# Performance work log

Measured on AMD Instinct MI355X. Metric: run time of the kernel, lower is better.

## Reference

```python
import jax, jax.numpy as jnp
import numpy as np

KER = 8  # patch size used by unfold/fold
EPS = 1e-5


def _gelu(x):
    return jax.nn.gelu(x, approximate=False)  # torch nn.GELU default (exact erf)


def _conv(x, w, b):
    # x: [B,C,H,W], w: [O,I,kh,kw]
    y = jax.lax.conv_general_dilated(x, w, (1, 1), 'SAME',
                                     dimension_numbers=('NCHW', 'OIHW', 'NCHW'))
    return y + b[None, :, None, None]


def _unfold_t(x):
    # F.unfold(k=8, s=8).transpose(1,2): [B,C,H,W] -> [B, L, C*k*k]
    B, C, H, W = x.shape
    Hp, Wp = H // KER, W // KER
    x = x.reshape(B, C, Hp, KER, Wp, KER)
    x = x.transpose(0, 2, 4, 1, 3, 5)  # [B,Hp,Wp,C,k,k]
    return x.reshape(B, Hp * Wp, C * KER * KER)


def _fold(y, H, W):
    # inverse of unfold (non-overlapping): [B,L,C*k*k] -> [B,C,H,W]
    B, L, D = y.shape
    Hp, Wp = H // KER, W // KER
    C = D // (KER * KER)
    y = y.reshape(B, Hp, Wp, C, KER, KER).transpose(0, 3, 1, 4, 2, 5)
    return y.reshape(B, C, H, W)


def _bn1d(x, gamma, beta):
    # BatchNorm1d (training-mode batch stats) on [B, C, L]: stats over (B, L)
    m = x.mean(axis=(0, 2), keepdims=True)
    v = x.var(axis=(0, 2), keepdims=True)  # biased variance, matches torch fwd
    return (x - m) * jax.lax.rsqrt(v + EPS) * gamma[None, :, None] + beta[None, :, None]


def setup_inputs() -> dict:
    key = jax.random.key(0)
    ks = jax.random.split(key, 12)
    B, C, H, W = 4, 64, 256, 256
    dq = KER * KER * C  # 4096

    def n(k, shape, scale=0.02):
        return jax.random.normal(k, shape, jnp.float32) * scale

    return {
        'feat': jax.random.normal(ks[0], (B, C, H, W), jnp.float32),
        'w_enc': n(ks[1], (C, C, 3, 3)), 'b_enc': jnp.zeros((C,), jnp.float32),
        'w_kc': n(ks[2], (C, C, 3, 3)), 'b_kc': jnp.zeros((C,), jnp.float32),
        'w_vc': n(ks[3], (C, C, 3, 3)), 'b_vc': jnp.zeros((C,), jnp.float32),
        'wq': n(ks[4], (1024, dq)), 'bq': jnp.zeros((1024,), jnp.float32),
        'wk': n(ks[5], (1024, dq)), 'bk': jnp.zeros((1024,), jnp.float32),
        'gq': jnp.ones((1024,), jnp.float32), 'betaq': jnp.zeros((1024,), jnp.float32),
        'gk': jnp.ones((1024,), jnp.float32), 'betak': jnp.zeros((1024,), jnp.float32),
        'w_f1': n(ks[6], (4 * C, C, 1, 1)), 'b_f1': jnp.zeros((4 * C,), jnp.float32),
        'w_f2': n(ks[7], (C, 4 * C, 1, 1)), 'b_f2': jnp.zeros((C,), jnp.float32),
    }


def reference(feat, w_enc, b_enc, w_kc, b_kc, w_vc, b_vc, wq, bq, wk, bk,
              gq, betaq, gk, betak, w_f1, b_f1, w_f2, b_f2):
    H, W = feat.shape[-2:]
    refer = _gelu(_conv(feat, w_enc, b_enc))
    feat_k = _gelu(_conv(feat, w_kc, b_kc))
    feat_v = _gelu(_conv(feat, w_vc, b_vc))

    q_un = _unfold_t(refer)   # [B,L,4096]
    k_un = _unfold_t(feat_k)
    v_un = _unfold_t(feat_v)

    # Linear -> BN1d over 1024 channels (transpose dance as in the torch code)
    qp = _bn1d((q_un @ wq.T + bq).transpose(0, 2, 1), gq, betaq).transpose(0, 2, 1)  # [B,L,1024]
    kp = _bn1d((k_un @ wk.T + bk).transpose(0, 2, 1), gk, betak).transpose(0, 2, 1)  # [B,L,1024]

    scale = jnp.sqrt(jnp.asarray(qp.shape[2], qp.dtype))
    scores = jnp.einsum('bld,bmd->blm', qp, kp) / scale  # [B,L,L]
    attn = jax.nn.softmax(scores, axis=2)
    out = jnp.einsum('blm,bmd->bld', attn, v_un)  # [B,L,4096]

    out = _fold(out, H, W)  # [B,C,H,W]
    ff = _gelu(_conv(out, w_f1, b_f1))
    ff = _gelu(_conv(ff, w_f2, b_f2))
    return ff + feat
```

## Files before the change

### kernel.cpp

```cpp
#include <hip/hip_runtime.h>
#include <hip/hip_bf16.h>

typedef unsigned short u16;
typedef __attribute__((ext_vector_type(8))) short short8v;
typedef __attribute__((ext_vector_type(8))) unsigned short u16x8;
typedef __attribute__((ext_vector_type(4))) float f32x4;

#define HWPIX 65536
#define AS1(p) ((const __attribute__((address_space(1))) void*)(p))
#define AS3(p) ((__attribute__((address_space(3))) void*)(p))

__device__ __forceinline__ float bfbits2f(u16 u) {
  return __uint_as_float(((unsigned)u) << 16);
}
__device__ __forceinline__ float4 ld4bf(const u16* p) {
  ushort4 u = *(const ushort4*)(const void*)p;
  return make_float4(bfbits2f(u.x), bfbits2f(u.y), bfbits2f(u.z), bfbits2f(u.w));
}
__device__ __forceinline__ u16 f2bf(float f) {
  union { __hip_bfloat16 h; u16 u; } c;
  c.h = __float2bfloat16(f);
  return c.u;
}
__device__ __forceinline__ float gelu_f(float x) {
  float z = 0.79788456f * x * (1.0f + 0.044715f * x * x);
  float e = __expf(2.0f * z);
  float th = 1.0f - 2.0f * __builtin_amdgcn_rcpf(e + 1.0f);
  return 0.5f * x * (1.0f + th);
}
__device__ __forceinline__ u16x8 bn8(u16x8 v, const float* __restrict__ sc,
                                     const float* __restrict__ sh, int kk) {
  float4 s0 = *(const float4*)&sc[kk], s1 = *(const float4*)&sc[kk + 4];
  float4 t0 = *(const float4*)&sh[kk], t1 = *(const float4*)&sh[kk + 4];
  u16x8 r;
  r[0] = f2bf(bfbits2f(v[0]) * s0.x + t0.x); r[1] = f2bf(bfbits2f(v[1]) * s0.y + t0.y);
  r[2] = f2bf(bfbits2f(v[2]) * s0.z + t0.z); r[3] = f2bf(bfbits2f(v[3]) * s0.w + t0.w);
  r[4] = f2bf(bfbits2f(v[4]) * s1.x + t1.x); r[5] = f2bf(bfbits2f(v[5]) * s1.y + t1.y);
  r[6] = f2bf(bfbits2f(v[6]) * s1.z + t1.z); r[7] = f2bf(bfbits2f(v[7]) * s1.w + t1.w);
  return r;
}

__launch_bounds__(256)
__global__ void nhwc_k(const float* __restrict__ x, u16* __restrict__ y) {
  __shared__ float tile[64][65];
  const int t = threadIdx.x;
  const int xs = blockIdx.x << 6, yy = blockIdx.y, b = blockIdx.z;
#pragma unroll
  for (int it = 0; it < 4; ++it) {
    const int idx = t + it * 256;
    const int c = idx >> 4, seg = (idx & 15) << 2;
    float4 v = *(const float4*)&x[(((size_t)(b * 64 + c)) << 16) + yy * 256 + xs + seg];
    tile[c][seg] = v.x; tile[c][seg + 1] = v.y; tile[c][seg + 2] = v.z; tile[c][seg + 3] = v.w;
  }
  __syncthreads();
#pragma unroll
  for (int it = 0; it < 4; ++it) {
    const int idx = t + it * 256;
    const int cs = (idx & 15) << 2, px = idx >> 4;
    ushort4 r;
    r.x = f2bf(tile[cs + 0][px]); r.y = f2bf(tile[cs + 1][px]);
    r.z = f2bf(tile[cs + 2][px]); r.w = f2bf(tile[cs + 3][px]);
    *(ushort4*)&y[(((size_t)((b * 256 + yy) * 256 + xs + px)) << 6) + cs] = r;
  }
}

__launch_bounds__(256)
__global__ void wcvt2_k(const float* __restrict__ s0, u16* __restrict__ d0,
                        const float* __restrict__ s1, u16* __restrict__ d1) {
  const float* src = blockIdx.y ? s1 : s0;
  u16* dst = blockIdx.y ? d1 : d0;
  const int i = (blockIdx.x * 256 + threadIdx.x) << 2;
  float4 v = *(const float4*)&src[i];
  ushort4 r;
  r.x = f2bf(v.x); r.y = f2bf(v.y); r.z = f2bf(v.z); r.w = f2bf(v.w);
  *(ushort4*)&dst[i] = r;
}

__launch_bounds__(256)
__global__ void wprep_k(const float* __restrict__ w0, const float* __restrict__ w1,
                        const float* __restrict__ w2, const float* __restrict__ b0,
                        const float* __restrict__ b1, const float* __restrict__ b2,
                        const float* __restrict__ wf1, const float* __restrict__ wf2,
                        u16* __restrict__ wT, float* __restrict__ bias192,
                        u16* __restrict__ wf1b, u16* __restrict__ wf2b) {
  const int t = threadIdx.x;
  const int bx = blockIdx.x;
  if (bx >= 497) {
    const int e = (bx - 497) * 256 + t;
    wf2b[e] = f2bf(wf2[e]);
    return;
  }
  if (bx >= 433) {
    const int e = (bx - 433) * 256 + t;
    wf1b[e] = f2bf(wf1[e]);
    return;
  }
  if (bx == 432) {
    if (t < 192) {
      const float* bp = (t < 64) ? b0 : (t < 128) ? b1 : b2;
      bias192[t] = bp[t & 63];
    }
    return;
  }
  const int e = bx * 256 + t;
  const int pos = e / 12288, rem = e % 12288;
  const int n = rem >> 6, ic = rem & 63;
  const int conv = n >> 6, oc = n & 63;
  const float* wp = (conv == 0) ? w0 : (conv == 1) ? w1 : w2;
  wT[e] = f2bf(wp[(oc * 64 + ic) * 9 + pos]);
}

__launch_bounds__(256)
__global__ void convmfma_k(const u16* __restrict__ featb, const u16* __restrict__ wT,
                           const float* __restrict__ bias192, u16* __restrict__ qun,
                           u16* __restrict__ kun, u16* __restrict__ vT) {
  __shared__ u16 As[128 * 64];
  __shared__ u16 Bs[192 * 64];
  const int tid = threadIdx.x;
  const int lin = blockIdx.x;
  const int virt = (lin & 7) * 256 + (lin >> 3);
  const int b = virt >> 9, yy = (virt >> 1) & 255, x0 = (virt & 1) << 7;
  const int lane = tid & 63, w = tid >> 6;
  const int wm = w >> 1, wn = w & 1;

  f32x4 acc[4][6] = {};
  const int kc = (lane >> 4) << 3;
  const int afr = wm * 64 + (lane & 15);
  const int bfr0 = wn * 96 + (lane & 15);

  for (int pos = 0; pos < 9; ++pos) {
    const int dy = pos / 3, dx = pos % 3;
    const int yp = yy + dy - 1;
    const bool yok = (unsigned)yp < 256u;
#pragma unroll
    for (int i = 0; i < 4; ++i) {
      const int slot = tid + (i << 8);
      const int row = slot >> 3, cg = slot & 7;
      const int xp = x0 + row + dx - 1;
      u16x8 v{};
      if (yok && (unsigned)xp < 256u)
        v = *(const u16x8*)&featb[(((size_t)((b * 256 + yp) * 256 + xp)) << 6) + (cg << 3)];
      *(u16x8*)&As[(row << 6) + ((cg ^ (row & 7)) << 3)] = v;
    }
    {
      const u16* wb = wT + (size_t)pos * 12288;
#pragma unroll
      for (int i = 0; i < 6; ++i) {
        const int slot = tid + (i << 8);
        const int row = slot >> 3, cg = slot & 7;
        *(u16x8*)&Bs[(row << 6) + ((cg ^ (row & 7)) << 3)] =
            *(const u16x8*)&wb[(row << 6) + (cg << 3)];
      }
    }
    __syncthreads();
#pragma unroll
    for (int ks = 0; ks < 2; ++ks) {
      const int ce = (ks << 5) + kc;
      short8v a[4], bf[6];
#pragma unroll
      for (int f = 0; f < 4; ++f) {
        const int row = afr + f * 16;
        a[f] = *(const short8v*)&As[(row << 6) + (ce ^ ((row & 7) << 3))];
      }
#pragma unroll
      for (int f = 0; f < 6; ++f) {
        const int row = bfr0 + f * 16;
        bf[f] = *(const short8v*)&Bs[(row << 6) + (ce ^ ((row & 7) << 3))];
      }
#pragma unroll
      for (int i = 0; i < 4; ++i)
#pragma unroll
        for (int j = 0; j < 6; ++j)
          acc[i][j] = __builtin_amdgcn_mfma_f32_16x16x32_bf16(a[i], bf[j], acc[i][j], 0, 0, 0);
    }
    __syncthreads();
  }

  const int py = yy >> 3, ky = yy & 7;
  const int rp0 = wm * 64 + ((lane >> 4) << 2);
#pragma unroll
  for (int j = 0; j < 6; ++j) {
    const int colb = wn * 96 + j * 16;
    const int conv = colb >> 6;
    const int oc = (colb & 63) + (lane & 15);
    const float bj = bias192[colb + (lane & 15)];
#pragma unroll
    for (int i = 0; i < 4; ++i) {
      const int rp = rp0 + i * 16;
      const int xg = x0 + rp;
      const int px = xg >> 3, kx0 = xg & 7;
      float v0 = gelu_f(acc[i][j][0] + bj);
      float v1 = gelu_f(acc[i][j][1] + bj);
      float v2 = gelu_f(acc[i][j][2] + bj);
      float v3 = gelu_f(acc[i][j][3] + bj);
      const int d0 = (oc << 6) + (ky << 3) + kx0;
      if (conv < 2) {
        u16* dst = conv ? kun : qun;
        const size_t addr = (((size_t)((b << 10) + py * 32 + px)) << 12) + d0;
        ushort4 r4;
        r4.x = f2bf(v0); r4.y = f2bf(v1); r4.z = f2bf(v2); r4.w = f2bf(v3);
        *(ushort4*)&dst[addr] = r4;
      } else {
        const int m = py * 32 + px;
        const size_t base = (((size_t)(b * 4096 + d0)) << 10) + m;
        vT[base] = f2bf(v0);
        vT[base + 1024] = f2bf(v1);
        vT[base + 2048] = f2bf(v2);
        vT[base + 3072] = f2bf(v3);
      }
    }
  }
}

__launch_bounds__(256)
__global__ void bnpart_k(const u16* __restrict__ q, const u16* __restrict__ k,
                         float2* __restrict__ part) {
  const u16* x = blockIdx.y ? k : q;
  const int b = blockIdx.x, t = threadIdx.x;
  const int c = t << 2;
  float s0 = 0.f, s1 = 0.f, s2 = 0.f, s3 = 0.f;
  float q0 = 0.f, q1 = 0.f, q2 = 0.f, q3 = 0.f;
  const u16* base = x + ((size_t)b << 15) + c;
#pragma unroll 4
  for (int r = 0; r < 32; ++r) {
    float4 v = ld4bf(base + (r << 10));
    s0 += v.x; q0 += v.x * v.x;
    s1 += v.y; q1 += v.y * v.y;
    s2 += v.z; q2 += v.z * v.z;
    s3 += v.w; q3 += v.w * v.w;
  }
  float2* dst = part + (((size_t)(blockIdx.y * 128 + b)) << 10) + c;
  dst[0] = make_float2(s0, q0);
  dst[1] = make_float2(s1, q1);
  dst[2] = make_float2(s2, q2);
  dst[3] = make_float2(s3, q3);
}
__launch_bounds__(256)
__global__ void bnfin_k(const float2* __restrict__ part, const float* __restrict__ gq,
                        const float* __restrict__ betaq, const float* __restrict__ gk,
                        const float* __restrict__ betak, float* __restrict__ scq,
                        float* __restrict__ shq, float* __restrict__ sck,
                        float* __restrict__ shk) {
  const int n = blockIdx.x * 256 + threadIdx.x;
  const int y = blockIdx.y;
  const float2* p = part + (((size_t)(y * 128)) << 10) + n;
  float S = 0.f, S2 = 0.f;
  for (int i = 0; i < 128; ++i) {
    float2 v = p[(size_t)i << 10];
    S += v.x; S2 += v.y;
  }
  const float mean = S * (1.0f / 4096.0f);
  const float var = S2 * (1.0f / 4096.0f) - mean * mean;
  const float rstd = rsqrtf(var + 1e-5f);
  const float g = (y ? gk : gq)[n];
  const float be = (y ? betak : betaq)[n];
  const float sc = g * rstd;
  (y ? sck : scq)[n] = sc;
  (y ? shk : shq)[n] = be - mean * sc;
}

__launch_bounds__(256)
__global__ void softmax_k(u16* __restrict__ s) {
  u16* p = s + (size_t)blockIdx.x * 1024;
  const int tid = threadIdx.x;
  float4 v = ld4bf(p + (tid << 2));
  float mx = fmaxf(fmaxf(v.x, v.y), fmaxf(v.z, v.w));
#pragma unroll
  for (int off = 32; off > 0; off >>= 1) mx = fmaxf(mx, __shfl_xor(mx, off));
  __shared__ float red[8];
  if ((tid & 63) == 0) red[tid >> 6] = mx;
  __syncthreads();
  mx = fmaxf(fmaxf(red[0], red[1]), fmaxf(red[2], red[3]));
  float e0 = __expf(v.x - mx), e1 = __expf(v.y - mx), e2 = __expf(v.z - mx), e3 = __expf(v.w - mx);
  float sm = e0 + e1 + e2 + e3;
#pragma unroll
  for (int off = 32; off > 0; off >>= 1) sm += __shfl_xor(sm, off);
  if ((tid & 63) == 0) red[4 + (tid >> 6)] = sm;
  __syncthreads();
  sm = red[4] + red[5] + red[6] + red[7];
  float inv = 1.0f / sm;
  ushort4 r;
  r.x = f2bf(e0 * inv); r.y = f2bf(e1 * inv); r.z = f2bf(e2 * inv); r.w = f2bf(e3 * inv);
  *(ushort4*)&p[tid << 2] = r;
}

template <int MODE>
__launch_bounds__(512)
__global__ void mgemmL_k(const u16* __restrict__ Ap0, const u16* __restrict__ Bp0,
                         const float* __restrict__ bias0, u16* __restrict__ Cp0, int K,
                         const u16* __restrict__ Ap2, const u16* __restrict__ Bp2,
                         const float* __restrict__ bias2, u16* __restrict__ Cp2) {
  constexpr int SD = (MODE == 0) ? 4096 : 1024;
  __shared__ u16 As[2][128 * 64];
  __shared__ u16 Bs[2][128 * 64];
  const int tid = threadIdx.x;

  int bx, by, z;
  if constexpr (MODE == 2) {
    int lin = blockIdx.x + 32 * blockIdx.y + 256 * blockIdx.z;
    int sw = (lin & 7) * 128 + (lin >> 3);
    bx = sw & 31; by = (sw >> 5) & 7; z = sw >> 8;
  } else {
    bx = blockIdx.x; by = blockIdx.y; z = blockIdx.z;
  }
  const u16* Ap = Ap0;
  const u16* Bp = Bp0;
  const float* bias = bias0;
  u16* Cp = Cp0;
  if constexpr (MODE == 0) {
    if (z) { Ap = Ap2; Bp = Bp2; bias = bias2; Cp = Cp2; }
  }
  const int m0 = by * 128, n0 = bx * 128;
  const int lane = tid & 63, w = tid >> 6;
  const int wm = w >> 2, wn = w & 3;

  const int srow = tid >> 3;
  const int scol = (((tid & 7) ^ (srow & 7)) << 3);
  const size_t zoffA = (MODE == 0) ? 0 : ((size_t)z << 10);
  const size_t zoffB = (MODE == 0) ? 0 : ((size_t)z << 12);
  const u16* gA0 = Ap + (zoffA + m0 + srow) * (size_t)SD + scol;
  const u16* gA1 = gA0 + (size_t)64 * SD;
  const u16* gB0 = Bp + (zoffB + n0 + srow) * (size_t)SD + scol;
  const u16* gB1 = gB0 + (size_t)64 * SD;
  const int lw0 = (w * 8) * 64;
  const int lw1 = (64 + w * 8) * 64;

  const int NT = K >> 6;
  __builtin_amdgcn_global_load_lds(AS1(gA0), AS3(&As[0][lw0]), 16, 0, 0);
  __builtin_amdgcn_global_load_lds(AS1(gA1), AS3(&As[0][lw1]), 16, 0, 0);
  __builtin_amdgcn_global_load_lds(AS1(gB0), AS3(&Bs[0][lw0]), 16, 0, 0);
  __builtin_amdgcn_global_load_lds(AS1(gB1), AS3(&Bs[0][lw1]), 16, 0, 0);

  f32x4 acc[4][2] = {};
  const int fr = lane & 15;
  const int kg = (lane >> 4) << 3;
  int cur = 0;
  for (int t = 0; t < NT; ++t) {
    __syncthreads();
    if (t + 1 < NT) {
      const int kn = (t + 1) << 6;
      __builtin_amdgcn_global_load_lds(AS1(gA0 + kn), AS3(&As[cur ^ 1][lw0]), 16, 0, 0);
      __builtin_amdgcn_global_load_lds(AS1(gA1 + kn), AS3(&As[cur ^ 1][lw1]), 16, 0, 0);
      __builtin_amdgcn_global_load_lds(AS1(gB0 + kn), AS3(&Bs[cur ^ 1][lw0]), 16, 0, 0);
      __builtin_amdgcn_global_load_lds(AS1(gB1 + kn), AS3(&Bs[cur ^ 1][lw1]), 16, 0, 0);
    }
    const u16* Asb = As[cur];
    const u16* Bsb = Bs[cur];
#pragma unroll
    for (int ks = 0; ks < 2; ++ks) {
      const int ce = ks * 32 + kg;
      short8v a[4], bfr[2];
#pragma unroll
      for (int f = 0; f < 4; ++f) {
        const int row = wm * 64 + fr + f * 16;
        a[f] = *(const short8v*)&Asb[row * 64 + (ce ^ ((row & 7) << 3))];
      }
#pragma unroll
      for (int f = 0; f < 2; ++f) {
        const int row = wn * 32 + fr + f * 16;
        bfr[f] = *(const short8v*)&Bsb[row * 64 + (ce ^ ((row & 7) << 3))];
      }
#pragma unroll
      for (int i = 0; i < 4; ++i)
#pragma unroll
        for (int j = 0; j < 2; ++j)
          acc[i][j] = __builtin_amdgcn_mfma_f32_16x16x32_bf16(a[i], bfr[j], acc[i][j], 0, 0, 0);
    }
    cur ^= 1;
  }

  const int rowbase = m0 + wm * 64 + ((lane >> 4) << 2);
  const int colbase = n0 + wn * 32 + (lane & 15);
  if constexpr (MODE == 2) {
    const size_t coff = (size_t)(8 + 8 * z) * 524288;
    u16* C = Cp + coff;
#pragma unroll
    for (int j = 0; j < 2; ++j) {
      const int d = colbase + j * 16;
      const int c = d >> 6, ky = (d >> 3) & 7, kx = d & 7;
#pragma unroll
      for (int i = 0; i < 4; ++i)
#pragma unroll
        for (int r = 0; r < 4; ++r) {
          const int l = rowbase + i * 16 + r;
          const int p = (((l >> 5) << 3) + ky) * 256 + ((l & 31) << 3) + kx;
          C[((size_t)p << 6) + c] = f2bf(acc[i][j][r]);
        }
    }
  } else {
#pragma unroll
    for (int j = 0; j < 2; ++j) {
      const int col = colbase + j * 16;
      const float bj = bias[col];
#pragma unroll
      for (int i = 0; i < 4; ++i)
#pragma unroll
        for (int r = 0; r < 4; ++r)
          Cp[(size_t)(rowbase + i * 16 + r) * 1024 + col] = f2bf(acc[i][j][r] + bj);
    }
  }
}

__launch_bounds__(512)
__global__ void mgemm1_k(const u16* __restrict__ Ap, const u16* __restrict__ Bp,
                         const float* __restrict__ sA, const float* __restrict__ hA,
                         const float* __restrict__ sB, const float* __restrict__ hB,
                         u16* __restrict__ Cp, int K) {
  constexpr int SD = 1024;
  __shared__ u16 As[2][128 * 72];
  __shared__ u16 Bs[2][128 * 72];
  const int tid = threadIdx.x;
  const int bx = blockIdx.x, by = blockIdx.y, z = blockIdx.z;
  const int m0 = by * 128, n0 = bx * 128;
  const int lane = tid & 63, w = tid >> 6;
  const int wm = w >> 2, wn = w & 3;

  const int srow = tid >> 3;
  const int scol = (tid & 7) << 3;
  const size_t zoff = (size_t)z << 10;
  const u16* A0 = Ap + (zoff + m0 + srow) * (size_t)SD + scol;
  const u16* A1 = A0 + (size_t)64 * SD;
  const u16* B0 = Bp + (zoff + n0 + srow) * (size_t)SD + scol;
  const u16* B1 = B0 + (size_t)64 * SD;
  const int l0 = srow * 72 + scol;
  const int l1 = (srow + 64) * 72 + scol;

  const int NT = K >> 6;
  u16x8 pA0 = bn8(*(const u16x8*)A0, sA, hA, scol);
  u16x8 pA1 = bn8(*(const u16x8*)A1, sA, hA, scol);
  u16x8 pB0 = bn8(*(const u16x8*)B0, sB, hB, scol);
  u16x8 pB1 = bn8(*(const u16x8*)B1, sB, hB, scol);
  *(u16x8*)&As[0][l0] = pA0; *(u16x8*)&As[0][l1] = pA1;
  *(u16x8*)&Bs[0][l0] = pB0; *(u16x8*)&Bs[0][l1] = pB1;
  __syncthreads();

  f32x4 acc[4][2] = {};
  int cur = 0;
  for (int t = 0; t < NT; ++t) {
    const int kn = (t + 1) << 6;
    if (t + 1 < NT) {
      pA0 = *(const u16x8*)(A0 + kn);
      pA1 = *(const u16x8*)(A1 + kn);
      pB0 = *(const u16x8*)(B0 + kn);
      pB1 = *(const u16x8*)(B1 + kn);
    }
    const u16* Asb = As[cur];
    const u16* Bsb = Bs[cur];
#pragma unroll
    for (int ks = 0; ks < 2; ++ks) {
      const int kc = ks * 32 + ((lane >> 4) << 3);
      short8v a[4], bfr[2];
#pragma unroll
      for (int f = 0; f < 4; ++f)
        a[f] = *(const short8v*)&Asb[(wm * 64 + (lane & 15) + f * 16) * 72 + kc];
#pragma unroll
      for (int f = 0; f < 2; ++f)
        bfr[f] = *(const short8v*)&Bsb[(wn * 32 + (lane & 15) + f * 16) * 72 + kc];
#pragma unroll
      for (int i = 0; i < 4; ++i)
#pragma unroll
        for (int j = 0; j < 2; ++j)
          acc[i][j] = __builtin_amdgcn_mfma_f32_16x16x32_bf16(a[i], bfr[j], acc[i][j], 0, 0, 0);
    }
    if (t + 1 < NT) {
      pA0 = bn8(pA0, sA, hA, kn + scol); pA1 = bn8(pA1, sA, hA, kn + scol);
      pB0 = bn8(pB0, sB, hB, kn + scol); pB1 = bn8(pB1, sB, hB, kn + scol);
      *(u16x8*)&As[cur ^ 1][l0] = pA0; *(u16x8*)&As[cur ^ 1][l1] = pA1;
      *(u16x8*)&Bs[cur ^ 1][l0] = pB0; *(u16x8*)&Bs[cur ^ 1][l1] = pB1;
    }
    __syncthreads();
    cur ^= 1;
  }

  const int rowbase = m0 + wm * 64 + ((lane >> 4) << 2);
  const int colbase = n0 + wn * 32 + (lane & 15);
#pragma unroll
  for (int j = 0; j < 2; ++j) {
    const int col = colbase + j * 16;
#pragma unroll
    for (int i = 0; i < 4; ++i)
#pragma unroll
      for (int r = 0; r < 4; ++r) {
        const size_t row = ((size_t)z << 10) + rowbase + i * 16 + r;
        Cp[row * 1024 + col] = f2bf(acc[i][j][r] * 0.03125f);
      }
  }
}

__launch_bounds__(512)
__global__ void ffn_k(const u16* __restrict__ fold, const u16* __restrict__ w1b,
                      const u16* __restrict__ w2b, const float* __restrict__ b1,
                      const float* __restrict__ b2, const float* __restrict__ feat,
                      float* __restrict__ out) {
  extern __shared__ u16 sh[];
  u16* Ash = sh;
  u16* W1s = sh + 9216;
  u16* mids = sh;
  const int t = threadIdx.x;
  const int px0 = blockIdx.x << 7;
  const int z = blockIdx.y;
  const u16* fz = fold + ((size_t)z << 22);

  {
    const int row = t >> 2, cs = (t & 3) << 4;
    const u16* src = fz + (((size_t)(px0 + row)) << 6) + cs;
    *(u16x8*)&Ash[row * 72 + cs] = *(const u16x8*)src;
    *(u16x8*)&Ash[row * 72 + cs + 8] = *(const u16x8*)(src + 8);
  }
  {
    const int row = t >> 1, cs = (t & 1) << 5;
    const u16* src = w1b + (((size_t)row) << 6) + cs;
    *(u16x8*)&W1s[row * 72 + cs] = *(const u16x8*)src;
    *(u16x8*)&W1s[row * 72 + cs + 8] = *(const u16x8*)(src + 8);
    *(u16x8*)&W1s[row * 72 + cs + 16] = *(const u16x8*)(src + 16);
    *(u16x8*)&W1s[row * 72 + cs + 24] = *(const u16x8*)(src + 24);
  }
  __syncthreads();

  const int lane = t & 63, w = t >> 6;
  const int kc = (lane >> 4) << 3;
  const int mrow = w * 16 + (lane & 15);
  f32x4 acc1[16] = {};
  short8v a0 = *(const short8v*)&Ash[mrow * 72 + kc];
  short8v a1 = *(const short8v*)&Ash[mrow * 72 + 32 + kc];
#pragma unroll
  for (int n = 0; n < 16; ++n) {
    const int br = n * 16 + (lane & 15);
    short8v b0 = *(const short8v*)&W1s[br * 72 + kc];
    short8v bv = *(const short8v*)&W1s[br * 72 + 32 + kc];
    acc1[n] = __builtin_amdgcn_mfma_f32_16x16x32_bf16(a0, b0, acc1[n], 0, 0, 0);
    acc1[n] = __builtin_amdgcn_mfma_f32_16x16x32_bf16(a1, bv, acc1[n], 0, 0, 0);
  }
  __syncthreads();

  const int mrow0 = w * 16 + ((lane >> 4) << 2);
#pragma unroll
  for (int n = 0; n < 16; ++n) {
    const int col = n * 16 + (lane & 15);
    const float bj = b1[col];
#pragma unroll
    for (int r = 0; r < 4; ++r)
      mids[(mrow0 + r) * 264 + col] = f2bf(gelu_f(acc1[n][r] + bj));
  }
  __syncthreads();

  f32x4 acc2[4] = {};
#pragma unroll
  for (int ks = 0; ks < 8; ++ks) {
    short8v a2 = *(const short8v*)&mids[(w * 16 + (lane & 15)) * 264 + ks * 32 + kc];
#pragma unroll
    for (int n = 0; n < 4; ++n) {
      short8v bv = *(const short8v*)(const void*)&w2b[(size_t)(n * 16 + (lane & 15)) * 256 + ks * 32 + kc];
      acc2[n] = __builtin_amdgcn_mfma_f32_16x16x32_bf16(a2, bv, acc2[n], 0, 0, 0);
    }
  }
#pragma unroll
  for (int n = 0; n < 4; ++n) {
    const int oc = n * 16 + (lane & 15);
    const float bn = b2[oc];
    const int px = px0 + mrow0;
    const size_t base = (((size_t)(z * 64 + oc)) << 16) + px;
    float4 f = *(const float4*)&feat[base];
    float4 rv;
    rv.x = gelu_f(acc2[n][0] + bn) + f.x;
    rv.y = gelu_f(acc2[n][1] + bn) + f.y;
    rv.z = gelu_f(acc2[n][2] + bn) + f.z;
    rv.w = gelu_f(acc2[n][3] + bn) + f.w;
    *(float4*)&out[base] = rv;
  }
}

extern "C" void kernel_launch(void* const* d_in, const int* in_sizes, int n_in,
                              void* d_out, int out_size, void* d_ws, size_t ws_size,
                              hipStream_t stream) {
  const float* feat  = (const float*)d_in[0];
  const float* w_enc = (const float*)d_in[1];
  const float* b_enc = (const float*)d_in[2];
  const float* w_kc  = (const float*)d_in[3];
  const float* b_kc  = (const float*)d_in[4];
  const float* w_vc  = (const float*)d_in[5];
  const float* b_vc  = (const float*)d_in[6];
  const float* wq    = (const float*)d_in[7];
  const float* bq    = (const float*)d_in[8];
  const float* wk    = (const float*)d_in[9];
  const float* bk    = (const float*)d_in[10];
  const float* gq    = (const float*)d_in[11];
  const float* betaq = (const float*)d_in[12];
  const float* gk    = (const float*)d_in[13];
  const float* betak = (const float*)d_in[14];
  const float* w_f1  = (const float*)d_in[15];
  const float* b_f1  = (const float*)d_in[16];
  const float* w_f2  = (const float*)d_in[17];
  const float* b_f2  = (const float*)d_in[18];

  char* ws = (char*)d_ws;
  const size_t MB = (size_t)1 << 20;
  u16*   qun    = (u16*)(ws);
  u16*   kun    = (u16*)(ws + 32 * MB);
  u16*   qlin   = (u16*)(ws + 64 * MB);
  u16*   klin   = (u16*)(ws + 40 * MB);
  u16*   wqb    = (u16*)(ws + 72 * MB);
  u16*   wT     = (u16*)(ws + 80 * MB);
  float* bias192= (float*)(ws + 80 * MB + 224 * 1024);
  float* scaleq = (float*)(ws + 80 * MB + 232 * 1024);
  float* shiftq = scaleq + 1024;
  float* scalek = shiftq + 1024;
  float* shiftk = scalek + 1024;
  u16*   wf1b   = (u16*)(ws + 80 * MB + 512 * 1024);
  u16*   wf2b   = (u16*)(ws + 80 * MB + 576 * 1024);
  float2* bnpart = (float2*)(ws + 81 * MB);
  u16*   scores = (u16*)(ws);
  u16*   featb  = (u16*)d_out;
  u16*   vT     = (u16*)((char*)d_out + 32 * MB);
  u16*   wkb    = (u16*)d_out;

  const dim3 blk(256);
  const dim3 blk8(512);
  nhwc_k<<<dim3(4, 256, 4), blk, 0, stream>>>(feat, featb);
  wprep_k<<<561, blk, 0, stream>>>(w_enc, w_kc, w_vc, b_enc, b_kc, b_vc,
                                   w_f1, w_f2, wT, bias192, wf1b, wf2b);
  convmfma_k<<<2048, blk, 0, stream>>>(featb, wT, bias192, qun, kun, vT);
  wcvt2_k<<<dim3(4096, 2), blk, 0, stream>>>(wq, wqb, wk, wkb);
  mgemmL_k<0><<<dim3(8, 32, 2), blk8, 0, stream>>>(qun, wqb, bq, qlin, 4096,
                                                   kun, wkb, bk, klin);
  bnpart_k<<<dim3(128, 2), blk, 0, stream>>>(qlin, klin, bnpart);
  bnfin_k<<<dim3(4, 2), blk, 0, stream>>>(bnpart, gq, betaq, gk, betak, scaleq, shiftq, scalek, shiftk);
  mgemm1_k<<<dim3(8, 8, 4), blk8, 0, stream>>>(qlin, klin, scaleq, shiftq, scalek, shiftk,
                                               scores, 1024);
  softmax_k<<<4096, blk, 0, stream>>>(scores);
  mgemmL_k<2><<<dim3(32, 8, 4), blk8, 0, stream>>>(scores, vT, nullptr, (u16*)ws, 1024,
                                                   nullptr, nullptr, nullptr, nullptr);
  ffn_k<<<dim3(512, 4), blk8, 67584, stream>>>((u16*)(ws + 8 * MB), wf1b, wf2b, b_f1, b_f2, feat, (float*)d_out);
  (void)in_sizes; (void)n_in; (void)out_size; (void)ws_size;
}
```

Measured before the change: 470.9 us.

## Merge prep kernels, register-prefetch conv tiles, relocate klin buffer

Merges the NHWC transpose and the weight-prep kernels into one launch to cut launch overhead. In the 3x3 conv MFMA kernel, the next tap's A/B tiles are now loaded into registers while the current tap's MFMAs run, then written to LDS after a barrier, so global latency overlaps compute. It also moves the klin buffer into the output region, which likely avoids aliasing with other workspace data. The prefetch adds register pressure (10 u16x8 vectors per thread) and an extra barrier per tap.

```diff
diff --git a/kernel.cpp b/kernel.cpp
--- a/kernel.cpp
+++ b/kernel.cpp
@@ -41,27 +41,61 @@
 }
 
 __launch_bounds__(256)
-__global__ void nhwc_k(const float* __restrict__ x, u16* __restrict__ y) {
+__global__ void prep_k(const float* __restrict__ feat, u16* __restrict__ featb,
+                       const float* __restrict__ w0, const float* __restrict__ w1,
+                       const float* __restrict__ w2, const float* __restrict__ b0,
+                       const float* __restrict__ b1, const float* __restrict__ b2,
+                       const float* __restrict__ wf1, const float* __restrict__ wf2,
+                       u16* __restrict__ wT, float* __restrict__ bias192,
+                       u16* __restrict__ wf1b, u16* __restrict__ wf2b) {
   __shared__ float tile[64][65];
   const int t = threadIdx.x;
-  const int xs = blockIdx.x << 6, yy = blockIdx.y, b = blockIdx.z;
-#pragma unroll
-  for (int it = 0; it < 4; ++it) {
-    const int idx = t + it * 256;
-    const int c = idx >> 4, seg = (idx & 15) << 2;
-    float4 v = *(const float4*)&x[(((size_t)(b * 64 + c)) << 16) + yy * 256 + xs + seg];
-    tile[c][seg] = v.x; tile[c][seg + 1] = v.y; tile[c][seg + 2] = v.z; tile[c][seg + 3] = v.w;
-  }
-  __syncthreads();
-#pragma unroll
-  for (int it = 0; it < 4; ++it) {
-    const int idx = t + it * 256;
-    const int cs = (idx & 15) << 2, px = idx >> 4;
-    ushort4 r;
-    r.x = f2bf(tile[cs + 0][px]); r.y = f2bf(tile[cs + 1][px]);
-    r.z = f2bf(tile[cs + 2][px]); r.w = f2bf(tile[cs + 3][px]);
-    *(ushort4*)&y[(((size_t)((b * 256 + yy) * 256 + xs + px)) << 6) + cs] = r;
-  }
+  const int bxg = blockIdx.x;
+  if (bxg < 4096) {
+    const int xs = (bxg & 3) << 6, yy = (bxg >> 2) & 255, b = bxg >> 10;
+#pragma unroll
+    for (int it = 0; it < 4; ++it) {
+      const int idx = t + it * 256;
+      const int c = idx >> 4, seg = (idx & 15) << 2;
+      float4 v = *(const float4*)&feat[(((size_t)(b * 64 + c)) << 16) + yy * 256 + xs + seg];
+      tile[c][seg] = v.x; tile[c][seg + 1] = v.y; tile[c][seg + 2] = v.z; tile[c][seg + 3] = v.w;
+    }
+    __syncthreads();
+#pragma unroll
+    for (int it = 0; it < 4; ++it) {
+      const int idx = t + it * 256;
+      const int cs = (idx & 15) << 2, px = idx >> 4;
+      ushort4 r;
+      r.x = f2bf(tile[cs + 0][px]); r.y = f2bf(tile[cs + 1][px]);
+      r.z = f2bf(tile[cs + 2][px]); r.w = f2bf(tile[cs + 3][px]);
+      *(ushort4*)&featb[(((size_t)((b * 256 + yy) * 256 + xs + px)) << 6) + cs] = r;
+    }
+    return;
+  }
+  const int bx = bxg - 4096;
+  if (bx >= 497) {
+    const int e = (bx - 497) * 256 + t;
+    wf2b[e] = f2bf(wf2[e]);
+    return;
+  }
+  if (bx >= 433) {
+    const int e = (bx - 433) * 256 + t;
+    wf1b[e] = f2bf(wf1[e]);
+    return;
+  }
+  if (bx == 432) {
+    if (t < 192) {
+      const float* bp = (t < 64) ? b0 : (t < 128) ? b1 : b2;
+      bias192[t] = bp[t & 63];
+    }
+    return;
+  }
+  const int e = bx * 256 + t;
+  const int pos = e / 12288, rem = e % 12288;
+  const int n = rem >> 6, ic = rem & 63;
+  const int conv = n >> 6, oc = n & 63;
+  const float* wp = (conv == 0) ? w0 : (conv == 1) ? w1 : w2;
+  wT[e] = f2bf(wp[(oc * 64 + ic) * 9 + pos]);
 }
 
 __launch_bounds__(256)
@@ -74,40 +108,6 @@
   ushort4 r;
   r.x = f2bf(v.x); r.y = f2bf(v.y); r.z = f2bf(v.z); r.w = f2bf(v.w);
   *(ushort4*)&dst[i] = r;
-}
-
-__launch_bounds__(256)
-__global__ void wprep_k(const float* __restrict__ w0, const float* __restrict__ w1,
-                        const float* __restrict__ w2, const float* __restrict__ b0,
-                        const float* __restrict__ b1, const float* __restrict__ b2,
-                        const float* __restrict__ wf1, const float* __restrict__ wf2,
-                        u16* __restrict__ wT, float* __restrict__ bias192,
-                        u16* __restrict__ wf1b, u16* __restrict__ wf2b) {
-  const int t = threadIdx.x;
-  const int bx = blockIdx.x;
-  if (bx >= 497) {
-    const int e = (bx - 497) * 256 + t;
-    wf2b[e] = f2bf(wf2[e]);
-    return;
-  }
-  if (bx >= 433) {
-    const int e = (bx - 433) * 256 + t;
-    wf1b[e] = f2bf(wf1[e]);
-    return;
-  }
-  if (bx == 432) {
-    if (t < 192) {
-      const float* bp = (t < 64) ? b0 : (t < 128) ? b1 : b2;
-      bias192[t] = bp[t & 63];
-    }
-    return;
-  }
-  const int e = bx * 256 + t;
-  const int pos = e / 12288, rem = e % 12288;
-  const int n = rem >> 6, ic = rem & 63;
-  const int conv = n >> 6, oc = n & 63;
-  const float* wp = (conv == 0) ? w0 : (conv == 1) ? w1 : w2;
-  wT[e] = f2bf(wp[(oc * 64 + ic) * 9 + pos]);
 }
 
 __launch_bounds__(256)
@@ -123,12 +123,8 @@
   const int lane = tid & 63, w = tid >> 6;
   const int wm = w >> 1, wn = w & 1;
 
-  f32x4 acc[4][6] = {};
-  const int kc = (lane >> 4) << 3;
-  const int afr = wm * 64 + (lane & 15);
-  const int bfr0 = wn * 96 + (lane & 15);
-
-  for (int pos = 0; pos < 9; ++pos) {
+  u16x8 rA[4], rB[6];
+  auto issue = [&](int pos) {
     const int dy = pos / 3, dx = pos % 3;
     const int yp = yy + dy - 1;
     const bool yok = (unsigned)yp < 256u;
@@ -140,19 +136,42 @@
       u16x8 v{};
       if (yok && (unsigned)xp < 256u)
         v = *(const u16x8*)&featb[(((size_t)((b * 256 + yp) * 256 + xp)) << 6) + (cg << 3)];
-      *(u16x8*)&As[(row << 6) + ((cg ^ (row & 7)) << 3)] = v;
-    }
-    {
-      const u16* wb = wT + (size_t)pos * 12288;
-#pragma unroll
-      for (int i = 0; i < 6; ++i) {
-        const int slot = tid + (i << 8);
-        const int row = slot >> 3, cg = slot & 7;
-        *(u16x8*)&Bs[(row << 6) + ((cg ^ (row & 7)) << 3)] =
-            *(const u16x8*)&wb[(row << 6) + (cg << 3)];
-      }
-    }
-    __syncthreads();
+      rA[i] = v;
+    }
+    const u16* wb = wT + (size_t)pos * 12288;
+#pragma unroll
+    for (int i = 0; i < 6; ++i) {
+      const int slot = tid + (i << 8);
+      const int row = slot >> 3, cg = slot & 7;
+      rB[i] = *(const u16x8*)&wb[(row << 6) + (cg << 3)];
+    }
+  };
+  auto commit = [&]() {
+#pragma unroll
+    for (int i = 0; i < 4; ++i) {
+      const int slot = tid + (i << 8);
+      const int row = slot >> 3, cg = slot & 7;
+      *(u16x8*)&As[(row << 6) + ((cg ^ (row & 7)) << 3)] = rA[i];
+    }
+#pragma unroll
+    for (int i = 0; i < 6; ++i) {
+      const int slot = tid + (i << 8);
+      const int row = slot >> 3, cg = slot & 7;
+      *(u16x8*)&Bs[(row << 6) + ((cg ^ (row & 7)) << 3)] = rB[i];
+    }
+  };
+
+  f32x4 acc[4][6] = {};
+  const int kc = (lane >> 4) << 3;
+  const int afr = wm * 64 + (lane & 15);
+  const int bfr0 = wn * 96 + (lane & 15);
+
+  issue(0);
+  commit();
+  __syncthreads();
+
+  for (int pos = 0; pos < 9; ++pos) {
+    if (pos + 1 < 9) issue(pos + 1);
 #pragma unroll
     for (int ks = 0; ks < 2; ++ks) {
       const int ce = (ks << 5) + kc;
@@ -174,6 +193,10 @@
           acc[i][j] = __builtin_amdgcn_mfma_f32_16x16x32_bf16(a[i], bf[j], acc[i][j], 0, 0, 0);
     }
     __syncthreads();
+    if (pos + 1 < 9) {
+      commit();
+      __syncthreads();
+    }
   }
 
   const int py = yy >> 3, ky = yy & 7;
@@ -598,7 +621,6 @@
   u16*   qun    = (u16*)(ws);
   u16*   kun    = (u16*)(ws + 32 * MB);
   u16*   qlin   = (u16*)(ws + 64 * MB);
-  u16*   klin   = (u16*)(ws + 40 * MB);
   u16*   wqb    = (u16*)(ws + 72 * MB);
   u16*   wT     = (u16*)(ws + 80 * MB);
   float* bias192= (float*)(ws + 80 * MB + 224 * 1024);
@@ -613,11 +635,11 @@
   u16*   featb  = (u16*)d_out;
   u16*   vT     = (u16*)((char*)d_out + 32 * MB);
   u16*   wkb    = (u16*)d_out;
+  u16*   klin   = (u16*)((char*)d_out + 8 * MB);
 
   const dim3 blk(256);
   const dim3 blk8(512);
-  nhwc_k<<<dim3(4, 256, 4), blk, 0, stream>>>(feat, featb);
-  wprep_k<<<561, blk, 0, stream>>>(w_enc, w_kc, w_vc, b_enc, b_kc, b_vc,
+  prep_k<<<4657, blk, 0, stream>>>(feat, featb, w_enc, w_kc, w_vc, b_enc, b_kc, b_vc,
                                    w_f1, w_f2, wT, bias192, wf1b, wf2b);
   convmfma_k<<<2048, blk, 0, stream>>>(featb, wT, bias192, qun, kun, vT);
   wcvt2_k<<<dim3(4096, 2), blk, 0, stream>>>(wq, wqb, wk, wkb);
```

Result: faster. 455.9 us (-3.2%).
